# Kernel tuning notes

Hardware: AMD Instinct MI355X
Metric: run time of the kernel (lower is better)

Reference implementation:

```python
import jax, jax.numpy as jnp
import numpy as np

N = 20000
E = 640000
R = 8          # num_rels == num_bases (basis regularizer with num_bases=-1)
B = 8
IN_SIZE = 128
HID = 256      # 4 * fea_dimen
FEA = 64
TIME = 2880
POI = 12


def setup_inputs() -> dict:
    key = jax.random.key(0)
    ks = jax.random.split(key, 20)
    s = 0.02
    inp = {
        'src': jax.random.randint(ks[0], (E,), 0, N),
        'dst': jax.random.randint(ks[1], (E,), 0, N),
        'etype': jax.random.randint(ks[2], (E,), 0, R),
        'poi_distribution': jax.random.normal(ks[3], (N, POI), jnp.float32),
        'time_distribution': jax.random.normal(ks[4], (N, TIME), jnp.float32),
        'road_feature': jax.random.normal(ks[5], (N, IN_SIZE), jnp.float32),
        # input projections
        'poi_w': jax.random.normal(ks[6], (POI, FEA), jnp.float32) * s,
        'poi_b': jnp.zeros((FEA,), jnp.float32),
        'time_w': jax.random.normal(ks[7], (TIME, 2 * FEA), jnp.float32) * s,
        'time_b': jnp.zeros((2 * FEA,), jnp.float32),
        'road_w': jax.random.normal(ks[8], (IN_SIZE, FEA), jnp.float32) * s,
        'road_b': jnp.zeros((FEA,), jnp.float32),
        # RelGraphConv layer 1 (basis decomposition)
        'basis1': jax.random.normal(ks[9], (B, HID, HID), jnp.float32) * s,
        'coef1': jax.random.normal(ks[10], (R, B), jnp.float32) * s,
        'loop_w1': jax.random.normal(ks[11], (HID, HID), jnp.float32) * s,
        'bias1': jnp.zeros((HID,), jnp.float32),
        # RelGraphConv layer 2
        'basis2': jax.random.normal(ks[12], (B, HID, HID), jnp.float32) * s,
        'coef2': jax.random.normal(ks[13], (R, B), jnp.float32) * s,
        'loop_w2': jax.random.normal(ks[14], (HID, HID), jnp.float32) * s,
        'bias2': jnp.zeros((HID,), jnp.float32),
    }
    return inp


def _rel_graph_conv(h, src, dst, etype, basis, coef, loop_w, bias):
    # W_r = sum_b coef[r,b] * basis[b]  -> (R, HID, HID), small
    W = jnp.einsum('rb,bio->rio', coef, basis)
    # transform every node by every relation weight, then gather per edge
    y = jnp.einsum('ni,rio->nro', h, W)          # (N, R, HID)
    msgs = y[src, etype]                          # (E, HID) gather
    agg = jax.ops.segment_sum(msgs, dst, num_segments=h.shape[0])  # scatter-sum
    return agg + h @ loop_w + bias


def reference(src, dst, etype, poi_distribution, time_distribution, road_feature,
              poi_w, poi_b, time_w, time_b, road_w, road_b,
              basis1, coef1, loop_w1, bias1, basis2, coef2, loop_w2, bias2):
    poi_feat = poi_distribution @ poi_w + poi_b       # (N, 64)
    time_feat = time_distribution @ time_w + time_b   # (N, 128)
    road_feat = road_feature @ road_w + road_b        # (N, 64)
    feat = jnp.concatenate([poi_feat, time_feat, road_feat], axis=1)  # (N, 256)
    h = _rel_graph_conv(feat, src, dst, etype, basis1, coef1, loop_w1, bias1)
    h = jax.nn.relu(h)  # dropout=0.0 -> identity
    h = _rel_graph_conv(h, src, dst, etype, basis2, coef2, loop_w2, bias2)
    return h
```

## Files before the change

kernel.cpp:

```cpp
#include <hip/hip_runtime.h>

#define NN 20000
#define NE 640000
#define NR 8
#define NB 8
#define HID 256
#define KPOI 12
#define KTIME 2880
#define KROAD 128
#define NK (NN * NR)
#define NS 9
#define KCAT (NS * HID)
#define SPLITK 5
#define KCH (KTIME / SPLITK)

typedef __attribute__((ext_vector_type(8))) short bf8_t;
typedef __attribute__((ext_vector_type(4))) float f4_t;

__device__ inline unsigned short f2bf(float f) {
  unsigned int u = __float_as_uint(f);
  u += 0x7FFF + ((u >> 16) & 1);
  return (unsigned short)(u >> 16);
}
__device__ inline float bf2f(unsigned short h) {
  return __uint_as_float((unsigned int)h << 16);
}

__global__ __launch_bounds__(256) void prep_k(
    const float* __restrict__ loop_w1, const float* __restrict__ loop_w2,
    const float* __restrict__ time_w,
    const float* __restrict__ coef1, const float* __restrict__ basis1,
    const float* __restrict__ coef2, const float* __restrict__ basis2,
    unsigned short* __restrict__ Wc1, unsigned short* __restrict__ Wc2,
    unsigned short* __restrict__ TWT)
{
  __shared__ unsigned short T[64][66];
  const int b = blockIdx.x;
  const int to = threadIdx.x & 63;
  const int tq = threadIdx.x >> 6;

  if (b < 256) {
    const int lr = b >> 4;
    const int tile = b & 15;
    const int i0 = ((tile >> 2) & 3) * 64, o0 = (tile & 3) * 64;
    const float* coef  = (lr < NR) ? coef1 : coef2;
    const float* basis = (lr < NR) ? basis1 : basis2;
    unsigned short* Wc = (lr < NR) ? Wc1 : Wc2;
    const int r = lr & 7;
    float cf[NB];
#pragma unroll
    for (int q = 0; q < NB; ++q) cf[q] = coef[r * NB + q];
#pragma unroll
    for (int k = 0; k < 16; ++k) {
      int i_loc = tq * 16 + k;
      int i = i0 + i_loc;
      float acc = 0.f;
#pragma unroll
      for (int q = 0; q < NB; ++q)
        acc += cf[q] * basis[((size_t)(q * HID + i)) * HID + o0 + to];
      T[i_loc][to] = f2bf(acc);
    }
    __syncthreads();
#pragma unroll
    for (int k = 0; k < 16; ++k) {
      int o_loc = tq * 16 + k;
      Wc[(size_t)(o0 + o_loc) * KCAT + r * HID + i0 + to] = T[to][o_loc];
    }
  } else if (b < 288) {
    const int j = b - 256;
    const int layer = j >> 4;
    const int tile = j & 15;
    const int i0 = ((tile >> 2) & 3) * 64, o0 = (tile & 3) * 64;
    const float* lw = layer ? loop_w2 : loop_w1;
    unsigned short* Wc = layer ? Wc2 : Wc1;
#pragma unroll
    for (int k = 0; k < 16; ++k) {
      int i_loc = tq * 16 + k;
      T[i_loc][to] = f2bf(lw[(size_t)(i0 + i_loc) * HID + o0 + to]);
    }
    __syncthreads();
#pragma unroll
    for (int k = 0; k < 16; ++k) {
      int o_loc = tq * 16 + k;
      Wc[(size_t)(o0 + o_loc) * KCAT + NR * HID + i0 + to] = T[to][o_loc];
    }
  } else {
    const int j = b - 288;
    const int r0 = (j >> 1) * 64, c0 = (j & 1) * 64;
#pragma unroll
    for (int k = 0; k < 16; ++k) {
      int r_loc = tq * 16 + k;
      T[r_loc][to] = f2bf(time_w[(size_t)(r0 + r_loc) * 128 + c0 + to]);
    }
    __syncthreads();
#pragma unroll
    for (int k = 0; k < 16; ++k) {
      int c_loc = tq * 16 + k;
      TWT[(size_t)(c0 + c_loc) * KTIME + r0 + to] = T[to][c_loc];
    }
  }
}

#define BK 16
__device__ inline void sgemm_body(
    int M, int Nn, int K,
    const float* __restrict__ A, int lda,
    const float* __restrict__ B, int ldb,
    const float* __restrict__ bias,
    unsigned short* __restrict__ C, int ldc, int brow)
{
  constexpr int BM = 64, BN = 64, TM = 4, TN = 4;
  constexpr int SA = BM + 4;
  constexpr int SB = BN + 4;
  __shared__ float As[BK * SA];
  __shared__ float Bs[BK * SB];
  const int tid = threadIdx.x;
  constexpr int TCOLS = BN / TN;
  const int row0 = (tid / TCOLS) * TM;
  const int col0 = (tid % TCOLS) * TN;

  float acc[TM][TN] = {};

  for (int kb = 0; kb < K; kb += BK) {
    {
      int i = tid;
      int r = i >> 2, q = (i & 3) * 4;
      int grow = brow + r, gk = kb + q;
      if (grow < M && gk + 3 < K) {
        float4 v = *(const float4*)(A + (size_t)grow * lda + gk);
        As[(q + 0) * SA + r] = v.x;
        As[(q + 1) * SA + r] = v.y;
        As[(q + 2) * SA + r] = v.z;
        As[(q + 3) * SA + r] = v.w;
      } else {
#pragma unroll
        for (int j = 0; j < 4; ++j)
          As[(q + j) * SA + r] =
              (grow < M && gk + j < K) ? A[(size_t)grow * lda + gk + j] : 0.f;
      }
    }
    {
      int i = tid;
      int k = i / (BN / 4), cq = (i % (BN / 4)) * 4;
      int gk = kb + k;
      float4 v = {0.f, 0.f, 0.f, 0.f};
      if (gk < K) {
        if (cq + 3 < Nn) {
          v = *(const float4*)(B + (size_t)gk * ldb + cq);
        } else {
#pragma unroll
          for (int j = 0; j < 4; ++j)
            if (cq + j < Nn) (&v.x)[j] = B[(size_t)gk * ldb + cq + j];
        }
      }
      *(float4*)(&Bs[k * SB + cq]) = v;
    }
    __syncthreads();
#pragma unroll
    for (int kk = 0; kk < BK; ++kk) {
      float a[TM], bb[TN];
      *(float4*)(&a[0]) = *(const float4*)(&As[kk * SA + row0]);
      *(float4*)(&bb[0]) = *(const float4*)(&Bs[kk * SB + col0]);
#pragma unroll
      for (int i = 0; i < TM; ++i)
#pragma unroll
        for (int j = 0; j < TN; ++j)
          acc[i][j] += a[i] * bb[j];
    }
    __syncthreads();
  }

  float bcache[TN];
#pragma unroll
  for (int j = 0; j < TN; ++j) bcache[j] = bias[col0 + j];
#pragma unroll
  for (int i = 0; i < TM; ++i) {
    int row = brow + row0 + i;
    if (row >= M) continue;
#pragma unroll
    for (int j = 0; j < TN; ++j)
      C[(size_t)row * ldc + col0 + j] = f2bf(acc[i][j] + bcache[j]);
  }
}

__global__ __launch_bounds__(256) void proj2_k(
    const float* __restrict__ poi_dist, const float* __restrict__ poi_w,
    const float* __restrict__ poi_b,
    const float* __restrict__ road_feat, const float* __restrict__ road_w,
    const float* __restrict__ road_b,
    unsigned short* __restrict__ hbuf)
{
  const int brow = blockIdx.x * 64;
  if (blockIdx.y == 0)
    sgemm_body(NN, 64, KPOI, poi_dist, KPOI, poi_w, 64, poi_b,
               hbuf + 0, HID, brow);
  else
    sgemm_body(NN, 64, KROAD, road_feat, KROAD, road_w, 64, road_b,
               hbuf + 192, HID, brow);
}

__global__ __launch_bounds__(256) void mfma_time_sk(
    const float* __restrict__ A,
    const unsigned short* __restrict__ BT,
    float* __restrict__ TP)
{
  __shared__ __align__(16) char ldsA[32 * 128];
  __shared__ __align__(16) char ldsB[128 * 128];
  const int tid = threadIdx.x;
  const int lane = tid & 63;
  const int w = tid >> 6;
  const int brow = blockIdx.x * 32;
  const int kb0 = blockIdx.y * KCH;

  f4_t acc[2][2];
#pragma unroll
  for (int i = 0; i < 2; ++i)
#pragma unroll
    for (int j = 0; j < 2; ++j) acc[i][j] = (f4_t){0.f, 0.f, 0.f, 0.f};

  for (int kb = kb0; kb < kb0 + KCH; kb += 64) {
    {
      int r = tid >> 3, c8 = tid & 7;
      const float* ap = A + (size_t)(brow + r) * KTIME + kb + c8 * 8;
      f4_t v0 = *(const f4_t*)ap;
      f4_t v1 = *(const f4_t*)(ap + 4);
      unsigned short hh[8];
#pragma unroll
      for (int j = 0; j < 4; ++j) { hh[j] = f2bf(v0[j]); hh[4 + j] = f2bf(v1[j]); }
      *(bf8_t*)(ldsA + r * 128 + ((c8 * 16) ^ ((r & 7) << 4))) = *(bf8_t*)hh;
    }
#pragma unroll
    for (int it = 0; it < 4; ++it) {
      int slot = tid + it * 256;
      int r = slot >> 3, c8 = slot & 7;
      bf8_t v = *(const bf8_t*)(BT + (size_t)r * KTIME + kb + c8 * 8);
      *(bf8_t*)(ldsB + r * 128 + ((c8 * 16) ^ ((r & 7) << 4))) = v;
    }
    __syncthreads();
#pragma unroll
    for (int ks = 0; ks < 2; ++ks) {
      const int kbyte = ks * 64 + (lane >> 4) * 16;
      bf8_t af[2], bfr[2];
#pragma unroll
      for (int mi = 0; mi < 2; ++mi) {
        int m = mi * 16 + (lane & 15);
        af[mi] = *(const bf8_t*)(ldsA + m * 128 + (kbyte ^ ((m & 7) << 4)));
      }
#pragma unroll
      for (int ni = 0; ni < 2; ++ni) {
        int n = w * 32 + ni * 16 + (lane & 15);
        bfr[ni] = *(const bf8_t*)(ldsB + n * 128 + (kbyte ^ ((n & 7) << 4)));
      }
#pragma unroll
      for (int mi = 0; mi < 2; ++mi)
#pragma unroll
        for (int ni = 0; ni < 2; ++ni)
          acc[mi][ni] = __builtin_amdgcn_mfma_f32_16x16x32_bf16(
              af[mi], bfr[ni], acc[mi][ni], 0, 0, 0);
    }
    __syncthreads();
  }

  float* tp = TP + (size_t)blockIdx.y * NN * 128;
  const int rq = (lane >> 4) * 4;
  const int cl = lane & 15;
#pragma unroll
  for (int ni = 0; ni < 2; ++ni) {
    int c = w * 32 + ni * 16 + cl;
#pragma unroll
    for (int mi = 0; mi < 2; ++mi) {
#pragma unroll
      for (int j = 0; j < 4; ++j) {
        int row = brow + mi * 16 + rq + j;
        tp[(size_t)row * 128 + c] = acc[mi][ni][j];
      }
    }
  }
}

__global__ __launch_bounds__(256) void time_finish(
    const float* __restrict__ TP, const float* __restrict__ bias,
    unsigned short* __restrict__ featb) {
  int i = blockIdx.x * 256 + threadIdx.x;
  if (i >= NN * 32) return;
  int row = i >> 5, c4 = (i & 31) * 4;
  f4_t s = *(const f4_t*)(TP + (size_t)row * 128 + c4);
#pragma unroll
  for (int k = 1; k < SPLITK; ++k) {
    f4_t v = *(const f4_t*)(TP + (size_t)k * NN * 128 + (size_t)row * 128 + c4);
    s.x += v.x; s.y += v.y; s.z += v.z; s.w += v.w;
  }
  f4_t b = *(const f4_t*)(bias + c4);
  unsigned short h[4] = {f2bf(s.x + b.x), f2bf(s.y + b.y),
                         f2bf(s.z + b.z), f2bf(s.w + b.w)};
  *(ushort4*)(featb + (size_t)row * 256 + 64 + c4) = *(ushort4*)h;
}

__global__ __launch_bounds__(256) void agg_k(
    const int* __restrict__ offs, const unsigned short* __restrict__ ssrc,
    const unsigned short* __restrict__ hin, unsigned short* __restrict__ Zc) {
  int w = (blockIdx.x * 256 + threadIdx.x) >> 6;
  int lane = threadIdx.x & 63;
  if (w >= NS * NN) return;
  int q = w / NN;
  int d = w - q * NN;
  unsigned short* zp = Zc + (size_t)d * KCAT + q * HID + lane * 4;
  if (q == NR) {
    *(ushort4*)zp = *(const ushort4*)(hin + (size_t)d * HID + lane * 4);
    return;
  }
  int lo = offs[d * NR + q];
  int hi = offs[d * NR + q + 1];
  f4_t az = {0.f, 0.f, 0.f, 0.f};
  int e = lo;
  for (; e + 4 <= hi; e += 4) {
    int s0 = ssrc[e], s1 = ssrc[e + 1], s2 = ssrc[e + 2], s3 = ssrc[e + 3];
    ushort4 u0 = *(const ushort4*)(hin + (size_t)s0 * HID + lane * 4);
    ushort4 u1 = *(const ushort4*)(hin + (size_t)s1 * HID + lane * 4);
    ushort4 u2 = *(const ushort4*)(hin + (size_t)s2 * HID + lane * 4);
    ushort4 u3 = *(const ushort4*)(hin + (size_t)s3 * HID + lane * 4);
    az.x += (bf2f(u0.x) + bf2f(u1.x)) + (bf2f(u2.x) + bf2f(u3.x));
    az.y += (bf2f(u0.y) + bf2f(u1.y)) + (bf2f(u2.y) + bf2f(u3.y));
    az.z += (bf2f(u0.z) + bf2f(u1.z)) + (bf2f(u2.z) + bf2f(u3.z));
    az.w += (bf2f(u0.w) + bf2f(u1.w)) + (bf2f(u2.w) + bf2f(u3.w));
  }
  for (; e < hi; ++e) {
    int s = ssrc[e];
    ushort4 u = *(const ushort4*)(hin + (size_t)s * HID + lane * 4);
    az.x += bf2f(u.x); az.y += bf2f(u.y);
    az.z += bf2f(u.z); az.w += bf2f(u.w);
  }
  unsigned short hz[4] = {f2bf(az.x), f2bf(az.y), f2bf(az.z), f2bf(az.w)};
  *(ushort4*)zp = *(ushort4*)hz;
}

template<int EPI>
__global__ __launch_bounds__(512) void gemm_cat(
    const unsigned short* __restrict__ Zc,
    const unsigned short* __restrict__ Wc,
    const float* __restrict__ bias,
    float* __restrict__ C, unsigned short* __restrict__ hb)
{
  __shared__ __align__(16) char At[64 * 128];
  __shared__ __align__(16) char Bt[256 * 128];
  const int tid = threadIdx.x;
  const int lane = tid & 63;
  const int w = tid >> 6;
  const int wm = w >> 2;
  const int wn = w & 3;
  const int brow = blockIdx.x * 64;

  f4_t acc[2][4];
#pragma unroll
  for (int i = 0; i < 2; ++i)
#pragma unroll
    for (int j = 0; j < 4; ++j) acc[i][j] = (f4_t){0.f, 0.f, 0.f, 0.f};

  for (int kb = 0; kb < KCAT; kb += 64) {
    {
      int r = tid >> 3, c8 = tid & 7;
      int grow = brow + r;
      bf8_t v = {0, 0, 0, 0, 0, 0, 0, 0};
      if (grow < NN) v = *(const bf8_t*)(Zc + (size_t)grow * KCAT + kb + c8 * 8);
      *(bf8_t*)(At + r * 128 + ((c8 * 16) ^ ((r & 7) << 4))) = v;
    }
#pragma unroll
    for (int it = 0; it < 4; ++it) {
      int slot = tid + it * 512;
      int n = slot >> 3, c8 = slot & 7;
      bf8_t v = *(const bf8_t*)(Wc + (size_t)n * KCAT + kb + c8 * 8);
      *(bf8_t*)(Bt + n * 128 + ((c8 * 16) ^ ((n & 7) << 4))) = v;
    }
    __syncthreads();
#pragma unroll
    for (int ks = 0; ks < 2; ++ks) {
      const int kbyte = ks * 64 + (lane >> 4) * 16;
      bf8_t af[2], bfr[4];
#pragma unroll
      for (int mi = 0; mi < 2; ++mi) {
        int m = wm * 32 + mi * 16 + (lane & 15);
        af[mi] = *(const bf8_t*)(At + m * 128 + (kbyte ^ ((m & 7) << 4)));
      }
#pragma unroll
      for (int ni = 0; ni < 4; ++ni) {
        int n = wn * 64 + ni * 16 + (lane & 15);
        bfr[ni] = *(const bf8_t*)(Bt + n * 128 + (kbyte ^ ((n & 7) << 4)));
      }
#pragma unroll
      for (int mi = 0; mi < 2; ++mi)
#pragma unroll
        for (int ni = 0; ni < 4; ++ni)
          acc[mi][ni] = __builtin_amdgcn_mfma_f32_16x16x32_bf16(
              af[mi], bfr[ni], acc[mi][ni], 0, 0, 0);
    }
    __syncthreads();
  }

  const int rq = (lane >> 4) * 4;
  const int cl = lane & 15;
#pragma unroll
  for (int ni = 0; ni < 4; ++ni) {
    int c = wn * 64 + ni * 16 + cl;
    float bv = bias[c];
#pragma unroll
    for (int mi = 0; mi < 2; ++mi) {
#pragma unroll
      for (int j = 0; j < 4; ++j) {
        int row = brow + wm * 32 + mi * 16 + rq + j;
        if (row < NN) {
          size_t o = (size_t)row * HID + c;
          float v = acc[mi][ni][j] + bv;
          if (EPI == 0) C[o] = v;
          else          hb[o] = f2bf(fmaxf(v, 0.f));
        }
      }
    }
  }
}

__global__ __launch_bounds__(256) void hist_k(const int* __restrict__ dst,
                                              const int* __restrict__ et,
                                              int* __restrict__ counts) {
  int e = blockIdx.x * 256 + threadIdx.x;
  if (e < NE) atomicAdd(&counts[dst[e] * NR + et[e]], 1);
}

__global__ __launch_bounds__(256) void scan_block(const int* __restrict__ counts,
                                                  int* __restrict__ offs,
                                                  int* __restrict__ bsums) {
  __shared__ int sh[256];
  int base = blockIdx.x * 1024;
  int t = threadIdx.x;
  int v[4];
  int s = 0;
#pragma unroll
  for (int j = 0; j < 4; ++j) {
    int idx = base + t * 4 + j;
    v[j] = (idx < NK) ? counts[idx] : 0;
    s += v[j];
  }
  sh[t] = s;
  __syncthreads();
  for (int off = 1; off < 256; off <<= 1) {
    int x = (t >= off) ? sh[t - off] : 0;
    __syncthreads();
    sh[t] += x;
    __syncthreads();
  }
  int run = sh[t] - s;
#pragma unroll
  for (int j = 0; j < 4; ++j) {
    int idx = base + t * 4 + j;
    if (idx < NK) offs[idx] = run;
    run += v[j];
  }
  if (t == 255) bsums[blockIdx.x] = sh[255];
}

__global__ __launch_bounds__(256) void scan_bsums(int* __restrict__ bsums, int nblk) {
  __shared__ int sh[256];
  int t = threadIdx.x;
  int own = (t < nblk) ? bsums[t] : 0;
  sh[t] = own;
  __syncthreads();
  for (int off = 1; off < 256; off <<= 1) {
    int x = (t >= off) ? sh[t - off] : 0;
    __syncthreads();
    sh[t] += x;
    __syncthreads();
  }
  int ex = sh[t] - own;
  if (t < nblk) bsums[t] = ex;
}

__global__ __launch_bounds__(256) void add_base(int* __restrict__ offs,
                                                const int* __restrict__ bsums,
                                                int* __restrict__ cursor) {
  int idx = blockIdx.x * 256 + threadIdx.x;
  if (idx < NK) {
    int v = offs[idx] + bsums[idx >> 10];
    offs[idx] = v;
    cursor[idx] = v;
  }
  if (idx == NK) offs[NK] = NE;
}

__global__ __launch_bounds__(256) void fill_k(const int* __restrict__ src,
                                              const int* __restrict__ dst,
                                              const int* __restrict__ et,
                                              int* __restrict__ cursor,
                                              unsigned short* __restrict__ ssrc) {
  int e = blockIdx.x * 256 + threadIdx.x;
  if (e < NE) {
    int key = dst[e] * NR + et[e];
    int p = atomicAdd(&cursor[key], 1);
    ssrc[p] = (unsigned short)src[e];
  }
}

extern "C" void kernel_launch(void* const* d_in, const int* in_sizes, int n_in,
                              void* d_out, int out_size, void* d_ws, size_t ws_size,
                              hipStream_t stream) {
  const int*   srcp      = (const int*)d_in[0];
  const int*   dstp      = (const int*)d_in[1];
  const int*   etypep    = (const int*)d_in[2];
  const float* poi_dist  = (const float*)d_in[3];
  const float* time_dist = (const float*)d_in[4];
  const float* road_feat = (const float*)d_in[5];
  const float* poi_w     = (const float*)d_in[6];
  const float* poi_b     = (const float*)d_in[7];
  const float* time_w    = (const float*)d_in[8];
  const float* time_b    = (const float*)d_in[9];
  const float* road_w    = (const float*)d_in[10];
  const float* road_b    = (const float*)d_in[11];
  const float* basis1    = (const float*)d_in[12];
  const float* coef1     = (const float*)d_in[13];
  const float* loop_w1   = (const float*)d_in[14];
  const float* bias1     = (const float*)d_in[15];
  const float* basis2    = (const float*)d_in[16];
  const float* coef2     = (const float*)d_in[17];
  const float* loop_w2   = (const float*)d_in[18];
  const float* bias2     = (const float*)d_in[19];

  float* out = (float*)d_out;

  char* ws = (char*)d_ws;
  unsigned short* Wc1    = (unsigned short*)(ws);
  unsigned short* Wc2    = (unsigned short*)(ws + 1179648);
  unsigned short* TWT    = (unsigned short*)(ws + 2359296);
  unsigned short* hbuf   = (unsigned short*)(ws + 3096576);
  unsigned short* Zcat   = (unsigned short*)(ws + 13336576);
  float*          TP     = (float*)(ws + 105496576);
  int*            offs   = (int*)  (ws + 156696576);
  int*            bsums  = (int*)  (ws + 157336592);
  unsigned short* ssrc   = (unsigned short*)(ws + 157337616);
  int*            counts = (int*)Zcat;
  int*            cursor = (int*)TP;

  dim3 blk(256);

  hipMemsetAsync(counts, 0, NK * sizeof(int), stream);
  hist_k<<<NE / 256, blk, 0, stream>>>(dstp, etypep, counts);
  scan_block<<<(NK + 1023) / 1024, blk, 0, stream>>>(counts, offs, bsums);
  scan_bsums<<<1, blk, 0, stream>>>(bsums, (NK + 1023) / 1024);
  add_base<<<(NK + 1 + 255) / 256, blk, 0, stream>>>(offs, bsums, cursor);
  fill_k<<<NE / 256, blk, 0, stream>>>(srcp, dstp, etypep, cursor, ssrc);

  prep_k<<<378, blk, 0, stream>>>(loop_w1, loop_w2, time_w,
                                  coef1, basis1, coef2, basis2,
                                  Wc1, Wc2, TWT);

  proj2_k<<<dim3((NN + 63) / 64, 2), blk, 0, stream>>>(
      poi_dist, poi_w, poi_b, road_feat, road_w, road_b, hbuf);
  mfma_time_sk<<<dim3(NN / 32, SPLITK), blk, 0, stream>>>(time_dist, TWT, TP);
  time_finish<<<(NN * 32 + 255) / 256, blk, 0, stream>>>(TP, time_b, hbuf);

  agg_k<<<(NS * NN + 3) / 4, blk, 0, stream>>>(offs, ssrc, hbuf, Zcat);
  gemm_cat<1><<<(NN + 63) / 64, 512, 0, stream>>>(Zcat, Wc1, bias1, nullptr, hbuf);

  agg_k<<<(NS * NN + 3) / 4, blk, 0, stream>>>(offs, ssrc, hbuf, Zcat);
  gemm_cat<0><<<(NN + 63) / 64, 512, 0, stream>>>(Zcat, Wc2, bias2, out, nullptr);
}
```

Measured before the change: 419.7 us.

## Fuse prep/projection kernels, in-block split-K time GEMM, single-pass scan, per-node aggregation

Merges weight preparation and the poi/road projections into one launch. Replaces the split-K time GEMM plus its reduction kernel with a 512-thread kernel that splits K across two wave groups and reduces through LDS, so the fp32 partial buffer is gone. Collapses the three scan kernels into one that uses a global counter spin-wait between blocks, which assumes all 157 blocks are resident at once. Aggregation now gives each wave one destination node and loops over all relations, replacing one wave per node-relation pair.

```diff
diff --git a/kernel.cpp b/kernel.cpp
--- a/kernel.cpp
+++ b/kernel.cpp
@@ -11,8 +11,6 @@
 #define NK (NN * NR)
 #define NS 9
 #define KCAT (NS * HID)
-#define SPLITK 5
-#define KCH (KTIME / SPLITK)
 
 typedef __attribute__((ext_vector_type(8))) short bf8_t;
 typedef __attribute__((ext_vector_type(4))) float f4_t;
@@ -24,81 +22,6 @@
 }
 __device__ inline float bf2f(unsigned short h) {
   return __uint_as_float((unsigned int)h << 16);
-}
-
-__global__ __launch_bounds__(256) void prep_k(
-    const float* __restrict__ loop_w1, const float* __restrict__ loop_w2,
-    const float* __restrict__ time_w,
-    const float* __restrict__ coef1, const float* __restrict__ basis1,
-    const float* __restrict__ coef2, const float* __restrict__ basis2,
-    unsigned short* __restrict__ Wc1, unsigned short* __restrict__ Wc2,
-    unsigned short* __restrict__ TWT)
-{
-  __shared__ unsigned short T[64][66];
-  const int b = blockIdx.x;
-  const int to = threadIdx.x & 63;
-  const int tq = threadIdx.x >> 6;
-
-  if (b < 256) {
-    const int lr = b >> 4;
-    const int tile = b & 15;
-    const int i0 = ((tile >> 2) & 3) * 64, o0 = (tile & 3) * 64;
-    const float* coef  = (lr < NR) ? coef1 : coef2;
-    const float* basis = (lr < NR) ? basis1 : basis2;
-    unsigned short* Wc = (lr < NR) ? Wc1 : Wc2;
-    const int r = lr & 7;
-    float cf[NB];
-#pragma unroll
-    for (int q = 0; q < NB; ++q) cf[q] = coef[r * NB + q];
-#pragma unroll
-    for (int k = 0; k < 16; ++k) {
-      int i_loc = tq * 16 + k;
-      int i = i0 + i_loc;
-      float acc = 0.f;
-#pragma unroll
-      for (int q = 0; q < NB; ++q)
-        acc += cf[q] * basis[((size_t)(q * HID + i)) * HID + o0 + to];
-      T[i_loc][to] = f2bf(acc);
-    }
-    __syncthreads();
-#pragma unroll
-    for (int k = 0; k < 16; ++k) {
-      int o_loc = tq * 16 + k;
-      Wc[(size_t)(o0 + o_loc) * KCAT + r * HID + i0 + to] = T[to][o_loc];
-    }
-  } else if (b < 288) {
-    const int j = b - 256;
-    const int layer = j >> 4;
-    const int tile = j & 15;
-    const int i0 = ((tile >> 2) & 3) * 64, o0 = (tile & 3) * 64;
-    const float* lw = layer ? loop_w2 : loop_w1;
-    unsigned short* Wc = layer ? Wc2 : Wc1;
-#pragma unroll
-    for (int k = 0; k < 16; ++k) {
-      int i_loc = tq * 16 + k;
-      T[i_loc][to] = f2bf(lw[(size_t)(i0 + i_loc) * HID + o0 + to]);
-    }
-    __syncthreads();
-#pragma unroll
-    for (int k = 0; k < 16; ++k) {
-      int o_loc = tq * 16 + k;
-      Wc[(size_t)(o0 + o_loc) * KCAT + NR * HID + i0 + to] = T[to][o_loc];
-    }
-  } else {
-    const int j = b - 288;
-    const int r0 = (j >> 1) * 64, c0 = (j & 1) * 64;
-#pragma unroll
-    for (int k = 0; k < 16; ++k) {
-      int r_loc = tq * 16 + k;
-      T[r_loc][to] = f2bf(time_w[(size_t)(r0 + r_loc) * 128 + c0 + to]);
-    }
-    __syncthreads();
-#pragma unroll
-    for (int k = 0; k < 16; ++k) {
-      int c_loc = tq * 16 + k;
-      TWT[(size_t)(c0 + c_loc) * KTIME + r0 + to] = T[to][c_loc];
-    }
-  }
 }
 
 #define BK 16
@@ -107,13 +30,13 @@
     const float* __restrict__ A, int lda,
     const float* __restrict__ B, int ldb,
     const float* __restrict__ bias,
-    unsigned short* __restrict__ C, int ldc, int brow)
+    unsigned short* __restrict__ C, int ldc, int brow, char* lds)
 {
   constexpr int BM = 64, BN = 64, TM = 4, TN = 4;
   constexpr int SA = BM + 4;
   constexpr int SB = BN + 4;
-  __shared__ float As[BK * SA];
-  __shared__ float Bs[BK * SB];
+  float* As = (float*)lds;
+  float* Bs = (float*)(lds + 4352);
   const int tid = threadIdx.x;
   constexpr int TCOLS = BN / TN;
   const int row0 = (tid / TCOLS) * TM;
@@ -183,34 +106,108 @@
   }
 }
 
-__global__ __launch_bounds__(256) void proj2_k(
+__global__ __launch_bounds__(256) void prep_proj_k(
+    const float* __restrict__ loop_w1, const float* __restrict__ loop_w2,
+    const float* __restrict__ time_w,
+    const float* __restrict__ coef1, const float* __restrict__ basis1,
+    const float* __restrict__ coef2, const float* __restrict__ basis2,
     const float* __restrict__ poi_dist, const float* __restrict__ poi_w,
     const float* __restrict__ poi_b,
     const float* __restrict__ road_feat, const float* __restrict__ road_w,
     const float* __restrict__ road_b,
-    unsigned short* __restrict__ hbuf)
+    unsigned short* __restrict__ Wc1, unsigned short* __restrict__ Wc2,
+    unsigned short* __restrict__ TWT, unsigned short* __restrict__ hbuf)
 {
-  const int brow = blockIdx.x * 64;
-  if (blockIdx.y == 0)
+  __shared__ __align__(16) char lds[8704];
+  const int b = blockIdx.x;
+  const int to = threadIdx.x & 63;
+  const int tq = threadIdx.x >> 6;
+
+  if (b < 378) {
+    unsigned short (*T)[66] = (unsigned short (*)[66])lds;
+    if (b < 256) {
+      const int lr = b >> 4;
+      const int tile = b & 15;
+      const int i0 = ((tile >> 2) & 3) * 64, o0 = (tile & 3) * 64;
+      const float* coef  = (lr < NR) ? coef1 : coef2;
+      const float* basis = (lr < NR) ? basis1 : basis2;
+      unsigned short* Wc = (lr < NR) ? Wc1 : Wc2;
+      const int r = lr & 7;
+      float cf[NB];
+#pragma unroll
+      for (int q = 0; q < NB; ++q) cf[q] = coef[r * NB + q];
+#pragma unroll
+      for (int k = 0; k < 16; ++k) {
+        int i_loc = tq * 16 + k;
+        int i = i0 + i_loc;
+        float acc = 0.f;
+#pragma unroll
+        for (int q = 0; q < NB; ++q)
+          acc += cf[q] * basis[((size_t)(q * HID + i)) * HID + o0 + to];
+        T[i_loc][to] = f2bf(acc);
+      }
+      __syncthreads();
+#pragma unroll
+      for (int k = 0; k < 16; ++k) {
+        int o_loc = tq * 16 + k;
+        Wc[(size_t)(o0 + o_loc) * KCAT + r * HID + i0 + to] = T[to][o_loc];
+      }
+    } else if (b < 288) {
+      const int j = b - 256;
+      const int layer = j >> 4;
+      const int tile = j & 15;
+      const int i0 = ((tile >> 2) & 3) * 64, o0 = (tile & 3) * 64;
+      const float* lw = layer ? loop_w2 : loop_w1;
+      unsigned short* Wc = layer ? Wc2 : Wc1;
+#pragma unroll
+      for (int k = 0; k < 16; ++k) {
+        int i_loc = tq * 16 + k;
+        T[i_loc][to] = f2bf(lw[(size_t)(i0 + i_loc) * HID + o0 + to]);
+      }
+      __syncthreads();
+#pragma unroll
+      for (int k = 0; k < 16; ++k) {
+        int o_loc = tq * 16 + k;
+        Wc[(size_t)(o0 + o_loc) * KCAT + NR * HID + i0 + to] = T[to][o_loc];
+      }
+    } else {
+      const int j = b - 288;
+      const int r0 = (j >> 1) * 64, c0 = (j & 1) * 64;
+#pragma unroll
+      for (int k = 0; k < 16; ++k) {
+        int r_loc = tq * 16 + k;
+        T[r_loc][to] = f2bf(time_w[(size_t)(r0 + r_loc) * 128 + c0 + to]);
+      }
+      __syncthreads();
+#pragma unroll
+      for (int k = 0; k < 16; ++k) {
+        int c_loc = tq * 16 + k;
+        TWT[(size_t)(c0 + c_loc) * KTIME + r0 + to] = T[to][c_loc];
+      }
+    }
+  } else if (b < 691) {
     sgemm_body(NN, 64, KPOI, poi_dist, KPOI, poi_w, 64, poi_b,
-               hbuf + 0, HID, brow);
-  else
+               hbuf + 0, HID, (b - 378) * 64, lds);
+  } else {
     sgemm_body(NN, 64, KROAD, road_feat, KROAD, road_w, 64, road_b,
-               hbuf + 192, HID, brow);
-}
-
-__global__ __launch_bounds__(256) void mfma_time_sk(
+               hbuf + 192, HID, (b - 691) * 64, lds);
+  }
+}
+
+__global__ __launch_bounds__(512) void mfma_time2(
     const float* __restrict__ A,
     const unsigned short* __restrict__ BT,
-    float* __restrict__ TP)
+    const float* __restrict__ bias,
+    unsigned short* __restrict__ featb)
 {
-  __shared__ __align__(16) char ldsA[32 * 128];
-  __shared__ __align__(16) char ldsB[128 * 128];
+  __shared__ __align__(16) char ldsA[2 * 32 * 128];
+  __shared__ __align__(16) char ldsB[2 * 128 * 128];
   const int tid = threadIdx.x;
   const int lane = tid & 63;
   const int w = tid >> 6;
+  const int g = w >> 2;
+  const int cb = w & 3;
   const int brow = blockIdx.x * 32;
-  const int kb0 = blockIdx.y * KCH;
 
   f4_t acc[2][2];
 #pragma unroll
@@ -218,120 +215,128 @@
 #pragma unroll
     for (int j = 0; j < 2; ++j) acc[i][j] = (f4_t){0.f, 0.f, 0.f, 0.f};
 
-  for (int kb = kb0; kb < kb0 + KCH; kb += 64) {
+  for (int i = 0; i < 23; ++i) {
     {
-      int r = tid >> 3, c8 = tid & 7;
-      const float* ap = A + (size_t)(brow + r) * KTIME + kb + c8 * 8;
-      f4_t v0 = *(const f4_t*)ap;
-      f4_t v1 = *(const f4_t*)(ap + 4);
-      unsigned short hh[8];
-#pragma unroll
-      for (int j = 0; j < 4; ++j) { hh[j] = f2bf(v0[j]); hh[4 + j] = f2bf(v1[j]); }
-      *(bf8_t*)(ldsA + r * 128 + ((c8 * 16) ^ ((r & 7) << 4))) = *(bf8_t*)hh;
+      int sg = tid >> 8, r = (tid >> 3) & 31, c8 = tid & 7;
+      int step = sg * 23 + i;
+      unsigned short hh[8] = {0, 0, 0, 0, 0, 0, 0, 0};
+      if (step < 45) {
+        const float* ap = A + (size_t)(brow + r) * KTIME + step * 64 + c8 * 8;
+        f4_t v0 = *(const f4_t*)ap;
+        f4_t v1 = *(const f4_t*)(ap + 4);
+#pragma unroll
+        for (int j = 0; j < 4; ++j) { hh[j] = f2bf(v0[j]); hh[4 + j] = f2bf(v1[j]); }
+      }
+      *(bf8_t*)(ldsA + sg * 4096 + r * 128 + ((c8 * 16) ^ ((r & 7) << 4))) =
+          *(bf8_t*)hh;
     }
 #pragma unroll
     for (int it = 0; it < 4; ++it) {
-      int slot = tid + it * 256;
-      int r = slot >> 3, c8 = slot & 7;
-      bf8_t v = *(const bf8_t*)(BT + (size_t)r * KTIME + kb + c8 * 8);
-      *(bf8_t*)(ldsB + r * 128 + ((c8 * 16) ^ ((r & 7) << 4))) = v;
-    }
-    __syncthreads();
-#pragma unroll
-    for (int ks = 0; ks < 2; ++ks) {
-      const int kbyte = ks * 64 + (lane >> 4) * 16;
-      bf8_t af[2], bfr[2];
+      int s = tid + it * 512;
+      int sg = s >> 10, r = (s >> 3) & 127, c8 = s & 7;
+      int step = sg * 23 + i;
+      bf8_t v = {0, 0, 0, 0, 0, 0, 0, 0};
+      if (step < 45)
+        v = *(const bf8_t*)(BT + (size_t)r * KTIME + step * 64 + c8 * 8);
+      *(bf8_t*)(ldsB + sg * 16384 + r * 128 + ((c8 * 16) ^ ((r & 7) << 4))) = v;
+    }
+    __syncthreads();
+    if (g * 23 + i < 45) {
+#pragma unroll
+      for (int ks = 0; ks < 2; ++ks) {
+        const int kbyte = ks * 64 + (lane >> 4) * 16;
+        bf8_t af[2], bfr[2];
+#pragma unroll
+        for (int mi = 0; mi < 2; ++mi) {
+          int m = mi * 16 + (lane & 15);
+          af[mi] = *(const bf8_t*)(
+              ldsA + g * 4096 + m * 128 + (kbyte ^ ((m & 7) << 4)));
+        }
+#pragma unroll
+        for (int ni = 0; ni < 2; ++ni) {
+          int n = cb * 32 + ni * 16 + (lane & 15);
+          bfr[ni] = *(const bf8_t*)(
+              ldsB + g * 16384 + n * 128 + (kbyte ^ ((n & 7) << 4)));
+        }
+#pragma unroll
+        for (int mi = 0; mi < 2; ++mi)
+#pragma unroll
+          for (int ni = 0; ni < 2; ++ni)
+            acc[mi][ni] = __builtin_amdgcn_mfma_f32_16x16x32_bf16(
+                af[mi], bfr[ni], acc[mi][ni], 0, 0, 0);
+      }
+    }
+    __syncthreads();
+  }
+
+  float* rb = (float*)ldsB;
+  if (g == 1) {
+#pragma unroll
+    for (int mi = 0; mi < 2; ++mi)
+#pragma unroll
+      for (int ni = 0; ni < 2; ++ni)
+#pragma unroll
+        for (int j = 0; j < 4; ++j)
+          rb[(cb * 64 + lane) * 16 + (mi * 2 + ni) * 4 + j] = acc[mi][ni][j];
+  }
+  __syncthreads();
+  if (g == 0) {
+    const int rq = (lane >> 4) * 4;
+    const int cl = lane & 15;
+#pragma unroll
+    for (int ni = 0; ni < 2; ++ni) {
+      int c = cb * 32 + ni * 16 + cl;
+      float bv = bias[c];
 #pragma unroll
       for (int mi = 0; mi < 2; ++mi) {
-        int m = mi * 16 + (lane & 15);
-        af[mi] = *(const bf8_t*)(ldsA + m * 128 + (kbyte ^ ((m & 7) << 4)));
-      }
-#pragma unroll
-      for (int ni = 0; ni < 2; ++ni) {
-        int n = w * 32 + ni * 16 + (lane & 15);
-        bfr[ni] = *(const bf8_t*)(ldsB + n * 128 + (kbyte ^ ((n & 7) << 4)));
-      }
-#pragma unroll
-      for (int mi = 0; mi < 2; ++mi)
-#pragma unroll
-        for (int ni = 0; ni < 2; ++ni)
-          acc[mi][ni] = __builtin_amdgcn_mfma_f32_16x16x32_bf16(
-              af[mi], bfr[ni], acc[mi][ni], 0, 0, 0);
-    }
-    __syncthreads();
-  }
-
-  float* tp = TP + (size_t)blockIdx.y * NN * 128;
-  const int rq = (lane >> 4) * 4;
-  const int cl = lane & 15;
-#pragma unroll
-  for (int ni = 0; ni < 2; ++ni) {
-    int c = w * 32 + ni * 16 + cl;
-#pragma unroll
-    for (int mi = 0; mi < 2; ++mi) {
-#pragma unroll
-      for (int j = 0; j < 4; ++j) {
-        int row = brow + mi * 16 + rq + j;
-        tp[(size_t)row * 128 + c] = acc[mi][ni][j];
-      }
-    }
-  }
-}
-
-__global__ __launch_bounds__(256) void time_finish(
-    const float* __restrict__ TP, const float* __restrict__ bias,
-    unsigned short* __restrict__ featb) {
-  int i = blockIdx.x * 256 + threadIdx.x;
-  if (i >= NN * 32) return;
-  int row = i >> 5, c4 = (i & 31) * 4;
-  f4_t s = *(const f4_t*)(TP + (size_t)row * 128 + c4);
-#pragma unroll
-  for (int k = 1; k < SPLITK; ++k) {
-    f4_t v = *(const f4_t*)(TP + (size_t)k * NN * 128 + (size_t)row * 128 + c4);
-    s.x += v.x; s.y += v.y; s.z += v.z; s.w += v.w;
-  }
-  f4_t b = *(const f4_t*)(bias + c4);
-  unsigned short h[4] = {f2bf(s.x + b.x), f2bf(s.y + b.y),
-                         f2bf(s.z + b.z), f2bf(s.w + b.w)};
-  *(ushort4*)(featb + (size_t)row * 256 + 64 + c4) = *(ushort4*)h;
+#pragma unroll
+        for (int j = 0; j < 4; ++j) {
+          float v = acc[mi][ni][j] +
+                    rb[(cb * 64 + lane) * 16 + (mi * 2 + ni) * 4 + j] + bv;
+          int row = brow + mi * 16 + rq + j;
+          featb[(size_t)row * 256 + 64 + c] = f2bf(v);
+        }
+      }
+    }
+  }
 }
 
 __global__ __launch_bounds__(256) void agg_k(
     const int* __restrict__ offs, const unsigned short* __restrict__ ssrc,
     const unsigned short* __restrict__ hin, unsigned short* __restrict__ Zc) {
-  int w = (blockIdx.x * 256 + threadIdx.x) >> 6;
+  int d = (blockIdx.x * 256 + threadIdx.x) >> 6;
   int lane = threadIdx.x & 63;
-  if (w >= NS * NN) return;
-  int q = w / NN;
-  int d = w - q * NN;
-  unsigned short* zp = Zc + (size_t)d * KCAT + q * HID + lane * 4;
-  if (q == NR) {
-    *(ushort4*)zp = *(const ushort4*)(hin + (size_t)d * HID + lane * 4);
-    return;
-  }
-  int lo = offs[d * NR + q];
-  int hi = offs[d * NR + q + 1];
-  f4_t az = {0.f, 0.f, 0.f, 0.f};
-  int e = lo;
-  for (; e + 4 <= hi; e += 4) {
-    int s0 = ssrc[e], s1 = ssrc[e + 1], s2 = ssrc[e + 2], s3 = ssrc[e + 3];
-    ushort4 u0 = *(const ushort4*)(hin + (size_t)s0 * HID + lane * 4);
-    ushort4 u1 = *(const ushort4*)(hin + (size_t)s1 * HID + lane * 4);
-    ushort4 u2 = *(const ushort4*)(hin + (size_t)s2 * HID + lane * 4);
-    ushort4 u3 = *(const ushort4*)(hin + (size_t)s3 * HID + lane * 4);
-    az.x += (bf2f(u0.x) + bf2f(u1.x)) + (bf2f(u2.x) + bf2f(u3.x));
-    az.y += (bf2f(u0.y) + bf2f(u1.y)) + (bf2f(u2.y) + bf2f(u3.y));
-    az.z += (bf2f(u0.z) + bf2f(u1.z)) + (bf2f(u2.z) + bf2f(u3.z));
-    az.w += (bf2f(u0.w) + bf2f(u1.w)) + (bf2f(u2.w) + bf2f(u3.w));
-  }
-  for (; e < hi; ++e) {
-    int s = ssrc[e];
-    ushort4 u = *(const ushort4*)(hin + (size_t)s * HID + lane * 4);
-    az.x += bf2f(u.x); az.y += bf2f(u.y);
-    az.z += bf2f(u.z); az.w += bf2f(u.w);
-  }
-  unsigned short hz[4] = {f2bf(az.x), f2bf(az.y), f2bf(az.z), f2bf(az.w)};
-  *(ushort4*)zp = *(ushort4*)hz;
+  if (d >= NN) return;
+  unsigned short* zrow = Zc + (size_t)d * KCAT;
+  *(ushort4*)(zrow + NR * HID + lane * 4) =
+      *(const ushort4*)(hin + (size_t)d * HID + lane * 4);
+  int ob[NR + 1];
+#pragma unroll
+  for (int r = 0; r <= NR; ++r) ob[r] = offs[d * NR + r];
+#pragma unroll 1
+  for (int q = 0; q < NR; ++q) {
+    int e = ob[q], hi = ob[q + 1];
+    f4_t az = {0.f, 0.f, 0.f, 0.f};
+    for (; e + 4 <= hi; e += 4) {
+      int s0 = ssrc[e], s1 = ssrc[e + 1], s2 = ssrc[e + 2], s3 = ssrc[e + 3];
+      ushort4 u0 = *(const ushort4*)(hin + (size_t)s0 * HID + lane * 4);
+      ushort4 u1 = *(const ushort4*)(hin + (size_t)s1 * HID + lane * 4);
+      ushort4 u2 = *(const ushort4*)(hin + (size_t)s2 * HID + lane * 4);
+      ushort4 u3 = *(const ushort4*)(hin + (size_t)s3 * HID + lane * 4);
+      az.x += (bf2f(u0.x) + bf2f(u1.x)) + (bf2f(u2.x) + bf2f(u3.x));
+      az.y += (bf2f(u0.y) + bf2f(u1.y)) + (bf2f(u2.y) + bf2f(u3.y));
+      az.z += (bf2f(u0.z) + bf2f(u1.z)) + (bf2f(u2.z) + bf2f(u3.z));
+      az.w += (bf2f(u0.w) + bf2f(u1.w)) + (bf2f(u2.w) + bf2f(u3.w));
+    }
+    for (; e < hi; ++e) {
+      int s = ssrc[e];
+      ushort4 u = *(const ushort4*)(hin + (size_t)s * HID + lane * 4);
+      az.x += bf2f(u.x); az.y += bf2f(u.y);
+      az.z += bf2f(u.z); az.w += bf2f(u.w);
+    }
+    unsigned short hz[4] = {f2bf(az.x), f2bf(az.y), f2bf(az.z), f2bf(az.w)};
+    *(ushort4*)(zrow + q * HID + lane * 4) = *(ushort4*)hz;
+  }
 }
 
 template<int EPI>
@@ -425,17 +430,20 @@
   if (e < NE) atomicAdd(&counts[dst[e] * NR + et[e]], 1);
 }
 
-__global__ __launch_bounds__(256) void scan_block(const int* __restrict__ counts,
-                                                  int* __restrict__ offs,
-                                                  int* __restrict__ bsums) {
+__global__ __launch_bounds__(256) void scan_all(
+    const int* __restrict__ counts, int* __restrict__ offs,
+    int* __restrict__ cursor, int* __restrict__ bsums,
+    int* __restrict__ counter) {
   __shared__ int sh[256];
-  int base = blockIdx.x * 1024;
-  int t = threadIdx.x;
-  int v[4];
+  __shared__ int base_sh;
+  const int bid = blockIdx.x;
+  const int t = threadIdx.x;
+  const int gbase = bid * 1024;
+  int v[4], run[4];
   int s = 0;
 #pragma unroll
   for (int j = 0; j < 4; ++j) {
-    int idx = base + t * 4 + j;
+    int idx = gbase + t * 4 + j;
     v[j] = (idx < NK) ? counts[idx] : 0;
     s += v[j];
   }
@@ -447,42 +455,35 @@
     sh[t] += x;
     __syncthreads();
   }
-  int run = sh[t] - s;
+  {
+    int r = sh[t] - s;
+#pragma unroll
+    for (int j = 0; j < 4; ++j) { run[j] = r; r += v[j]; }
+  }
+  if (t == 255) {
+    bsums[bid] = sh[255];
+    __threadfence();
+    atomicAdd(counter, 1);
+  }
+  if (t == 0) {
+    while (atomicAdd(counter, 0) < (int)gridDim.x) {}
+    __threadfence();
+    int b = 0;
+    for (int j = 0; j < bid; ++j) b += atomicAdd(&bsums[j], 0);
+    base_sh = b;
+  }
+  __syncthreads();
+  const int base = base_sh;
 #pragma unroll
   for (int j = 0; j < 4; ++j) {
-    int idx = base + t * 4 + j;
-    if (idx < NK) offs[idx] = run;
-    run += v[j];
-  }
-  if (t == 255) bsums[blockIdx.x] = sh[255];
-}
-
-__global__ __launch_bounds__(256) void scan_bsums(int* __restrict__ bsums, int nblk) {
-  __shared__ int sh[256];
-  int t = threadIdx.x;
-  int own = (t < nblk) ? bsums[t] : 0;
-  sh[t] = own;
-  __syncthreads();
-  for (int off = 1; off < 256; off <<= 1) {
-    int x = (t >= off) ? sh[t - off] : 0;
-    __syncthreads();
-    sh[t] += x;
-    __syncthreads();
-  }
-  int ex = sh[t] - own;
-  if (t < nblk) bsums[t] = ex;
-}
-
-__global__ __launch_bounds__(256) void add_base(int* __restrict__ offs,
-                                                const int* __restrict__ bsums,
-                                                int* __restrict__ cursor) {
-  int idx = blockIdx.x * 256 + threadIdx.x;
-  if (idx < NK) {
-    int v = offs[idx] + bsums[idx >> 10];
-    offs[idx] = v;
-    cursor[idx] = v;
-  }
-  if (idx == NK) offs[NK] = NE;
+    int idx = gbase + t * 4 + j;
+    if (idx < NK) {
+      int val = run[j] + base;
+      offs[idx] = val;
+      cursor[idx] = val;
+    }
+  }
+  if (bid == 0 && t == 0) offs[NK] = NE;
 }
 
 __global__ __launch_bounds__(256) void fill_k(const int* __restrict__ src,
@@ -530,34 +531,32 @@
   unsigned short* TWT    = (unsigned short*)(ws + 2359296);
   unsigned short* hbuf   = (unsigned short*)(ws + 3096576);
   unsigned short* Zcat   = (unsigned short*)(ws + 13336576);
-  float*          TP     = (float*)(ws + 105496576);
-  int*            offs   = (int*)  (ws + 156696576);
-  int*            bsums  = (int*)  (ws + 157336592);
-  unsigned short* ssrc   = (unsigned short*)(ws + 157337616);
+  int*            offs   = (int*)  (ws + 105496576);
+  int*            bsums  = (int*)  (ws + 106136592);
+  unsigned short* ssrc   = (unsigned short*)(ws + 106137616);
+  int*            cursor = (int*)  (ws + 107417616);
   int*            counts = (int*)Zcat;
-  int*            cursor = (int*)TP;
+  int*            counter = counts + NK;
 
   dim3 blk(256);
 
-  hipMemsetAsync(counts, 0, NK * sizeof(int), stream);
+  hipMemsetAsync(counts, 0, (NK + 1) * sizeof(int), stream);
   hist_k<<<NE / 256, blk, 0, stream>>>(dstp, etypep, counts);
-  scan_block<<<(NK + 1023) / 1024, blk, 0, stream>>>(counts, offs, bsums);
-  scan_bsums<<<1, blk, 0, stream>>>(bsums, (NK + 1023) / 1024);
-  add_base<<<(NK + 1 + 255) / 256, blk, 0, stream>>>(offs, bsums, cursor);
+  scan_all<<<(NK + 1023) / 1024, blk, 0, stream>>>(counts, offs, cursor,
+                                                   bsums, counter);
   fill_k<<<NE / 256, blk, 0, stream>>>(srcp, dstp, etypep, cursor, ssrc);
 
-  prep_k<<<378, blk, 0, stream>>>(loop_w1, loop_w2, time_w,
-                                  coef1, basis1, coef2, basis2,
-                                  Wc1, Wc2, TWT);
-
-  proj2_k<<<dim3((NN + 63) / 64, 2), blk, 0, stream>>>(
-      poi_dist, poi_w, poi_b, road_feat, road_w, road_b, hbuf);
-  mfma_time_sk<<<dim3(NN / 32, SPLITK), blk, 0, stream>>>(time_dist, TWT, TP);
-  time_finish<<<(NN * 32 + 255) / 256, blk, 0, stream>>>(TP, time_b, hbuf);
-
-  agg_k<<<(NS * NN + 3) / 4, blk, 0, stream>>>(offs, ssrc, hbuf, Zcat);
+  prep_proj_k<<<1004, blk, 0, stream>>>(loop_w1, loop_w2, time_w,
+                                        coef1, basis1, coef2, basis2,
+                                        poi_dist, poi_w, poi_b,
+                                        road_feat, road_w, road_b,
+                                        Wc1, Wc2, TWT, hbuf);
+
+  mfma_time2<<<NN / 32, 512, 0, stream>>>(time_dist, TWT, time_b, hbuf);
+
+  agg_k<<<NN * 64 / 256, blk, 0, stream>>>(offs, ssrc, hbuf, Zcat);
   gemm_cat<1><<<(NN + 63) / 64, 512, 0, stream>>>(Zcat, Wc1, bias1, nullptr, hbuf);
 
-  agg_k<<<(NS * NN + 3) / 4, blk, 0, stream>>>(offs, ssrc, hbuf, Zcat);
+  agg_k<<<NN * 64 / 256, blk, 0, stream>>>(offs, ssrc, hbuf, Zcat);
   gemm_cat<0><<<(NN + 63) / 64, 512, 0, stream>>>(Zcat, Wc2, bias2, out, nullptr);
 }
```

After: 399.5 us. 4.8% less time.
